# Optimization experiments

Hardware: AMD Instinct MI355X
Metric: run time of the kernel (lower is better)

Reference implementation:

```python
import jax, jax.numpy as jnp
import numpy as np

B, S, D, H, DH, TLEN, TD = 4, 1024, 1024, 16, 64, 256, 256
EPS = 1e-5


def layer_norm(x, g, b):
    m = jnp.mean(x, axis=-1, keepdims=True)
    v = jnp.mean((x - m) ** 2, axis=-1, keepdims=True)
    return (x - m) * jax.lax.rsqrt(v + EPS) * g + b


def rotate_half(x):
    x1, x2 = jnp.split(x, 2, axis=-1)
    return jnp.concatenate((-x2, x1), axis=-1)


def apply_rope(pos, t):
    # pos: [S, DH] -> [1, S, 1, DH]; t: [B, S, H, DH]
    p = pos[None, :, None, :]
    return t * jnp.cos(p) + rotate_half(t) * jnp.sin(p)


def mha(q_in, kv_in, in_w, in_b, out_w, out_b, n_heads):
    # standard nn.MultiheadAttention math (batch-first tensors here)
    d = q_in.shape[-1]
    dh = d // n_heads
    q = q_in @ in_w[:d].T + in_b[:d]
    k = kv_in @ in_w[d:2 * d].T + in_b[d:2 * d]
    v = kv_in @ in_w[2 * d:].T + in_b[2 * d:]
    q = q.reshape(q.shape[0], q.shape[1], n_heads, dh)
    k = k.reshape(k.shape[0], k.shape[1], n_heads, dh)
    v = v.reshape(v.shape[0], v.shape[1], n_heads, dh)
    scores = jnp.einsum('bihd,bjhd->bhij', q, k) / jnp.sqrt(jnp.asarray(dh, q.dtype))
    attn = jax.nn.softmax(scores, axis=-1)
    o = jnp.einsum('bhij,bjhd->bihd', attn, v)
    o = o.reshape(o.shape[0], o.shape[1], d)
    return o @ out_w.T + out_b


def setup_inputs():
    key = jax.random.key(0)
    ks = jax.random.split(key, 20)
    s = 0.02
    inp = {
        'x': jax.random.normal(ks[0], (B, S, D), jnp.float32),
        'text_emb': jax.random.normal(ks[1], (B, TLEN, D), jnp.float32),
        'time_emb': jax.random.normal(ks[2], (B, TD), jnp.float32),
    }
    # true RoPE position encoding, matching RotaryEmbedding.forward
    inv_freq = 1.0 / (10000 ** (jnp.arange(0, DH, 2, dtype=jnp.float32) / DH))
    freqs = jnp.arange(S, dtype=jnp.float32)[:, None] * inv_freq[None, :]
    inp['rotary_pos'] = jnp.concatenate((freqs, freqs), axis=-1)  # [S, DH]
    inp.update(
        ln1_g=jnp.ones((D,), jnp.float32), ln1_b=jnp.zeros((D,), jnp.float32),
        ln2_g=jnp.ones((D,), jnp.float32), ln2_b=jnp.zeros((D,), jnp.float32),
        ln3_g=jnp.ones((D,), jnp.float32), ln3_b=jnp.zeros((D,), jnp.float32),
        attn_in_w=jax.random.normal(ks[3], (3 * D, D), jnp.float32) * s,
        attn_in_b=jnp.zeros((3 * D,), jnp.float32),
        ca_in_w=jax.random.normal(ks[4], (3 * D, D), jnp.float32) * s,
        ca_in_b=jnp.zeros((3 * D,), jnp.float32),
        ca_out_w=jax.random.normal(ks[5], (D, D), jnp.float32) * s,
        ca_out_b=jnp.zeros((D,), jnp.float32),
        fc1_w=jax.random.normal(ks[6], (4 * D, D), jnp.float32) * s,
        fc1_b=jnp.zeros((4 * D,), jnp.float32),
        gate_w=jax.random.normal(ks[7], (4 * D, D), jnp.float32) * s,
        gate_b=jnp.zeros((4 * D,), jnp.float32),
        fc2_w=jax.random.normal(ks[8], (D, 4 * D), jnp.float32) * s,
        fc2_b=jnp.zeros((D,), jnp.float32),
    )
    return inp


def reference(x, text_emb, time_emb, rotary_pos,
              ln1_g, ln1_b, ln2_g, ln2_b, ln3_g, ln3_b,
              attn_in_w, attn_in_b,
              ca_in_w, ca_in_b, ca_out_w, ca_out_b,
              fc1_w, fc1_b, gate_w, gate_b, fc2_w, fc2_b):
    b, n, d = x.shape
    # --- self-attention with manual RoPE (NOTE: original skips out_proj) ---
    residual = x
    xn = layer_norm(x, ln1_g, ln1_b)
    q = xn @ attn_in_w[:d].T + attn_in_b[:d]
    k = xn @ attn_in_w[d:2 * d].T + attn_in_b[d:2 * d]
    v = xn @ attn_in_w[2 * d:].T + attn_in_b[2 * d:]
    q = q.reshape(b, n, H, DH)
    k = k.reshape(b, n, H, DH)
    v = v.reshape(b, n, H, DH)
    q = apply_rope(rotary_pos, q)
    k = apply_rope(rotary_pos, k)
    scores = jnp.einsum('bihd,bjhd->bhij', q, k) / jnp.sqrt(jnp.asarray(DH, x.dtype))
    attn = jax.nn.softmax(scores, axis=-1)
    attn_out = jnp.einsum('bhij,bjhd->bihd', attn, v).reshape(b, n, d)
    x = attn_out + residual
    # --- cross-attention (full MHA, dropout inactive at eval) ---
    residual = x
    xn = layer_norm(x, ln2_g, ln2_b)
    x = mha(xn, text_emb, ca_in_w, ca_in_b, ca_out_w, ca_out_b, H) + residual
    # --- gated MLP ---
    residual = x
    xn = layer_norm(x, ln3_g, ln3_b)
    h = jax.nn.gelu(xn @ fc1_w.T + fc1_b, approximate=False)
    g = jax.nn.sigmoid(xn @ gate_w.T + gate_b)
    return (h * g) @ fc2_w.T + fc2_b + residual
```

## Files before the change

kernel.cpp:

```cpp
#include <hip/hip_runtime.h>
#include <hip/hip_bf16.h>

#define SEQ 1024
#define DIM 1024
#define NH 16

typedef __bf16 bf16_t;
typedef __bf16 bf16x8 __attribute__((ext_vector_type(8)));
typedef __bf16 bf16x4 __attribute__((ext_vector_type(4)));
typedef float f32x4 __attribute__((ext_vector_type(4)));

__device__ __forceinline__ f32x4 mfma16(bf16x8 a, bf16x8 b, f32x4 c) {
    return __builtin_amdgcn_mfma_f32_16x16x32_bf16(a, b, c, 0, 0, 0);
}

__device__ __forceinline__ void gload16(const bf16_t* g, bf16_t* l) {
    __builtin_amdgcn_global_load_lds(
        (const __attribute__((address_space(1))) void*)g,
        (__attribute__((address_space(3))) void*)l, 16, 0, 0);
}

enum { EPI_BF16 = 0, EPI_F32_RESID = 1 };

__global__ __launch_bounds__(256) void cvt_kernel(const float* __restrict__ in,
                                                  bf16_t* __restrict__ out) {
    const int i = blockIdx.x * 256 + threadIdx.x;
    const float4 v = ((const float4*)in)[i];
    bf16x4 o = {(bf16_t)v.x, (bf16_t)v.y, (bf16_t)v.z, (bf16_t)v.w};
    ((bf16x4*)out)[i] = o;
}

__global__ __launch_bounds__(256) void ln_kernel(const float* __restrict__ in,
                                                 const float* __restrict__ g,
                                                 const float* __restrict__ bsh,
                                                 bf16_t* __restrict__ out) {
    __shared__ float red[4], red2[4];
    const int row = blockIdx.x, tid = threadIdx.x;
    const float4 v = ((const float4*)(in + (size_t)row * DIM))[tid];
    float s = v.x + v.y + v.z + v.w;
#pragma unroll
    for (int o = 32; o; o >>= 1) s += __shfl_down(s, o, 64);
    if ((tid & 63) == 0) red[tid >> 6] = s;
    __syncthreads();
    const float mean = (red[0] + red[1] + red[2] + red[3]) * (1.0f / DIM);
    const float dx = v.x - mean, dy = v.y - mean, dz = v.z - mean, dw = v.w - mean;
    float s2 = dx * dx + dy * dy + dz * dz + dw * dw;
#pragma unroll
    for (int o = 32; o; o >>= 1) s2 += __shfl_xor(s2, o, 64);
    if ((tid & 63) == 0) red2[tid >> 6] = s2;
    __syncthreads();
    const float var = (red2[0] + red2[1] + red2[2] + red2[3]) * (1.0f / DIM);
    const float rs = rsqrtf(var + 1e-5f);
    const float4 gv = ((const float4*)g)[tid];
    const float4 bv = ((const float4*)bsh)[tid];
    bf16x4 o4 = {(bf16_t)(dx * rs * gv.x + bv.x), (bf16_t)(dy * rs * gv.y + bv.y),
                 (bf16_t)(dz * rs * gv.z + bv.z), (bf16_t)(dw * rs * gv.w + bv.w)};
    ((bf16x4*)(out + (size_t)row * DIM))[tid] = o4;
}

__global__ __launch_bounds__(256) void rope_kernel(bf16_t* __restrict__ qkv,
                                                   const float* __restrict__ rp) {
    const int t = blockIdx.x * 256 + threadIdx.x;
    const int row = t >> 9;
    const int rem = t & 511;
    const int h = rem >> 5, d = rem & 31;
    const int s = row & (SEQ - 1);
    const float p0 = rp[s * 64 + d];
    const float p1 = rp[s * 64 + d + 32];
    float s0, c0, s1, c1;
    sincosf(p0, &s0, &c0);
    sincosf(p1, &s1, &c1);
    const size_t base = (size_t)row * 3072 + h * 64 + d;
#pragma unroll
    for (int off = 0; off <= 1024; off += 1024) {
        const float a = (float)qkv[base + off];
        const float b = (float)qkv[base + off + 32];
        qkv[base + off] = (bf16_t)(a * c0 - b * s0);
        qkv[base + off + 32] = (bf16_t)(b * c1 + a * s1);
    }
}

__device__ __forceinline__ float epi_apply_gelu(float v) {
    return 0.5f * v * (1.0f + erff(v * 0.70710678118f));
}

__global__ __launch_bounds__(256) void vtrans_kernel(
    const bf16_t* __restrict__ src, int ld, int voff, int skv,
    bf16_t* __restrict__ vt) {
    __shared__ bf16_t T[64 * 72];
    const int qt = blockIdx.x, h = blockIdx.y, b = blockIdx.z;
    const int tid = threadIdx.x;
    const int s0 = qt * 64;
#pragma unroll
    for (int t = 0; t < 2; ++t) {
        const int idx = t * 256 + tid;
        const int r = idx >> 3, c8 = (idx & 7) * 8;
        bf16x8 v = *(const bf16x8*)(src + (size_t)(b * skv + s0 + r) * ld +
                                    voff + h * 64 + c8);
        *(bf16x8*)&T[r * 72 + c8] = v;
    }
    __syncthreads();
    const size_t base = ((size_t)(b * NH + h) * 64) * skv;
#pragma unroll
    for (int t = 0; t < 2; ++t) {
        const int idx = t * 256 + tid;
        const int d = idx >> 3, s8 = (idx & 7) * 8;
        bf16x8 w;
#pragma unroll
        for (int i = 0; i < 8; ++i) w[i] = T[(s8 + i) * 72 + d];
        *(bf16x8*)(vt + base + (size_t)d * skv + s0 + s8) = w;
    }
}

#define ALD 72
template <bool OUTBF>
__global__ __launch_bounds__(256) void attn2_kernel(
    const bf16_t* __restrict__ qp, int ldq, int qoff,
    const bf16_t* __restrict__ kp, int ldk, int koff,
    const bf16_t* __restrict__ vtp, int skv,
    const float* __restrict__ resid, void* __restrict__ outp, float scale) {
    __shared__ bf16_t Ks[4096];
    __shared__ bf16_t Vs[4096];
    __shared__ bf16_t Ps[4 * 16 * ALD];
    const int nwg = gridDim.x;
    const int t = (blockIdx.x & 7) * (nwg >> 3) + (blockIdx.x >> 3);
    const int qt = t & 15;
    const int bh = t >> 4;
    const int b = bh >> 4, h = bh & 15;
    const int tid = threadIdx.x;
    const int wave = tid >> 6, lane = tid & 63;
    const int lr = lane & 15, hi = lane >> 4;

    const size_t qrow = (size_t)(b * SEQ + qt * 64 + wave * 16 + lr);
    const bf16_t* qb = qp + qrow * ldq + qoff + h * 64;
    const bf16x8 qf0 = *(const bf16x8*)(qb + hi * 8);
    const bf16x8 qf1 = *(const bf16x8*)(qb + 32 + hi * 8);

    const bf16_t* vbase = vtp + ((size_t)bh * 64) * skv;

    f32x4 oacc[4];
#pragma unroll
    for (int n = 0; n < 4; ++n) oacc[n] = (f32x4){0.f, 0.f, 0.f, 0.f};
    float mrun[4] = {-1e30f, -1e30f, -1e30f, -1e30f};
    float lrun[4] = {0.f, 0.f, 0.f, 0.f};

    bf16_t* pw = &Ps[wave * 16 * ALD];
    const int nkt = skv >> 6;
    for (int kt = 0; kt < nkt; ++kt) {
#pragma unroll
        for (int u = 0; u < 2; ++u) {
            const int c = wave * 2 + u;
            const int grow = wave * 16 + lr, gcol = u * 32 + hi * 8;
            gload16(kp + (size_t)(b * skv + kt * 64 + grow) * ldk + koff +
                        h * 64 + gcol,
                    &Ks[c * 512]);
            gload16(vbase + (size_t)grow * skv + kt * 64 + gcol, &Vs[c * 512]);
        }
        __syncthreads();

        f32x4 s[4];
#pragma unroll
        for (int n = 0; n < 4; ++n) {
            f32x4 z = (f32x4){0.f, 0.f, 0.f, 0.f};
            z = mfma16(qf0, *(const bf16x8*)&Ks[(n * 2 + 0) * 512 + hi * 128 + lr * 8], z);
            z = mfma16(qf1, *(const bf16x8*)&Ks[(n * 2 + 1) * 512 + hi * 128 + lr * 8], z);
            s[n] = z * scale;
        }
        float alpha[4];
#pragma unroll
        for (int j = 0; j < 4; ++j) {
            float mt = fmaxf(fmaxf(s[0][j], s[1][j]), fmaxf(s[2][j], s[3][j]));
#pragma unroll
            for (int o = 8; o >= 1; o >>= 1) mt = fmaxf(mt, __shfl_xor(mt, o, 64));
            const float mnew = fmaxf(mrun[j], mt);
            alpha[j] = __expf(mrun[j] - mnew);
            float rsum = 0.f;
#pragma unroll
            for (int n = 0; n < 4; ++n) {
                const float p = __expf(s[n][j] - mnew);
                s[n][j] = p;
                rsum += p;
            }
#pragma unroll
            for (int o = 8; o >= 1; o >>= 1) rsum += __shfl_xor(rsum, o, 64);
            lrun[j] = lrun[j] * alpha[j] + rsum;
            mrun[j] = mnew;
        }
#pragma unroll
        for (int j = 0; j < 4; ++j) {
            const int pr = hi * 4 + j;
#pragma unroll
            for (int n = 0; n < 4; ++n) pw[pr * ALD + n * 16 + lr] = (bf16_t)s[n][j];
        }
#pragma unroll
        for (int n = 0; n < 4; ++n)
#pragma unroll
            for (int j = 0; j < 4; ++j) oacc[n][j] *= alpha[j];
#pragma unroll
        for (int ks = 0; ks < 2; ++ks) {
            const bf16x8 pa = *(const bf16x8*)&pw[lr * ALD + ks * 32 + hi * 8];
#pragma unroll
            for (int n = 0; n < 4; ++n) {
                const bf16x8 vf =
                    *(const bf16x8*)&Vs[(n * 2 + ks) * 512 + hi * 128 + lr * 8];
                oacc[n] = mfma16(pa, vf, oacc[n]);
            }
        }
        __syncthreads();
    }

    const size_t orow0 = (size_t)(b * SEQ + qt * 64 + wave * 16);
#pragma unroll
    for (int n = 0; n < 4; ++n) {
#pragma unroll
        for (int j = 0; j < 4; ++j) {
            const int r = hi * 4 + j;
            const size_t idx = (orow0 + r) * DIM + h * 64 + n * 16 + lr;
            float val = oacc[n][j] / lrun[j];
            if constexpr (OUTBF) {
                ((bf16_t*)outp)[idx] = (bf16_t)val;
            } else {
                ((float*)outp)[idx] = val + resid[idx];
            }
        }
    }
}

template <int EPI, int MODE>
__global__ __launch_bounds__(512, 4) void gemm8w(
    const bf16_t* __restrict__ A, int lda, const bf16_t* __restrict__ W, int ldw,
    const float* __restrict__ bias, const void* __restrict__ aux,
    void* __restrict__ outv, int ldo, int K, int nM) {
    __shared__ bf16_t As[2][8192];
    __shared__ bf16_t Bs[2][8192];
    const int tid = threadIdx.x;
    const int wave = tid >> 6, lane = tid & 63;
    const int wm = wave >> 2, wn = wave & 3;
    const int lr = lane & 15, hi = lane >> 4;

    const int x = blockIdx.x & 7, i = blockIdx.x >> 3;
    int mt, nt;
    if constexpr (MODE == 0) {
        const int mc = nM >> 3;
        mt = x * mc + (i % mc);
        nt = i / mc;
    } else {
        const int nc = (gridDim.x / nM) >> 3;
        nt = x * nc + (i % nc);
        mt = i / nc;
    }
    const int rowA0 = mt * 128, rowB0 = nt * 128;

    f32x4 acc[4][2];
#pragma unroll
    for (int m = 0; m < 4; ++m)
#pragma unroll
        for (int n = 0; n < 2; ++n) acc[m][n] = (f32x4){0.f, 0.f, 0.f, 0.f};

    auto stage = [&](int kt, int b) {
        const int k0 = kt * 64;
#pragma unroll
        for (int u = 0; u < 2; ++u) {
            const int c = wave * 2 + u;
            const int grow = wave * 16 + lr, gcol = k0 + u * 32 + hi * 8;
            gload16(A + (size_t)(rowA0 + grow) * lda + gcol, &As[b][c * 512]);
            gload16(W + (size_t)(rowB0 + grow) * ldw + gcol, &Bs[b][c * 512]);
        }
    };

    const int NT = K >> 6;
    stage(0, 0);
    stage(1, 1);
    asm volatile("s_waitcnt vmcnt(4)" ::: "memory");
    __builtin_amdgcn_s_barrier();

    for (int kt = 0; kt < NT; ++kt) {
        const int cur = kt & 1;
#pragma unroll
        for (int ks = 0; ks < 2; ++ks) {
            bf16x8 af[4], bfr[2];
#pragma unroll
            for (int mf = 0; mf < 4; ++mf)
                af[mf] = *(const bf16x8*)&As[cur][((wm * 4 + mf) * 2 + ks) * 512 +
                                                 hi * 128 + lr * 8];
#pragma unroll
            for (int nf = 0; nf < 2; ++nf)
                bfr[nf] = *(const bf16x8*)&Bs[cur][((wn * 2 + nf) * 2 + ks) * 512 +
                                                  hi * 128 + lr * 8];
#pragma unroll
            for (int mf = 0; mf < 4; ++mf)
#pragma unroll
                for (int nf = 0; nf < 2; ++nf)
                    acc[mf][nf] = mfma16(af[mf], bfr[nf], acc[mf][nf]);
        }
        if (kt + 1 < NT) {
            __builtin_amdgcn_sched_barrier(0);
            __builtin_amdgcn_s_barrier();
            if (kt + 2 < NT) {
                stage(kt + 2, cur);
                asm volatile("s_waitcnt vmcnt(4)" ::: "memory");
            } else {
                asm volatile("s_waitcnt vmcnt(0)" ::: "memory");
            }
            __builtin_amdgcn_s_barrier();
        }
    }

    float bn[2];
#pragma unroll
    for (int n = 0; n < 2; ++n) bn[n] = bias[rowB0 + wn * 32 + n * 16 + lr];
#pragma unroll
    for (int m = 0; m < 4; ++m) {
#pragma unroll
        for (int j = 0; j < 4; ++j) {
            const int row = rowA0 + wm * 64 + m * 16 + hi * 4 + j;
#pragma unroll
            for (int n = 0; n < 2; ++n) {
                const int col = rowB0 + wn * 32 + n * 16 + lr;
                float val = acc[m][n][j] + bn[n];
                const size_t oidx = (size_t)row * ldo + col;
                if constexpr (EPI == EPI_BF16) {
                    ((bf16_t*)outv)[oidx] = (bf16_t)val;
                } else {
                    ((float*)outv)[oidx] = val + ((const float*)aux)[oidx];
                }
            }
        }
    }
}

__global__ __launch_bounds__(512, 4) void gemm_mlp(
    const bf16_t* __restrict__ A, int lda, const bf16_t* __restrict__ W1,
    const bf16_t* __restrict__ Wg, int ldw, const float* __restrict__ b1,
    const float* __restrict__ bg, bf16_t* __restrict__ outv, int ldo, int K,
    int nM) {
    __shared__ bf16_t As[2][8192];
    __shared__ bf16_t Bs[2][8192];
    const int tid = threadIdx.x;
    const int wave = tid >> 6, lane = tid & 63;
    const int wm = wave >> 2, wn = wave & 3;
    const int lr = lane & 15, hi = lane >> 4;

    const int x = blockIdx.x & 7, i = blockIdx.x >> 3;
    const int nc = (gridDim.x / nM) >> 3;
    const int nt = x * nc + (i % nc), mt = i / nc;
    const int rowA0 = mt * 128, colB0 = nt * 64;

    f32x4 acc[4][2];
#pragma unroll
    for (int m = 0; m < 4; ++m)
#pragma unroll
        for (int n = 0; n < 2; ++n) acc[m][n] = (f32x4){0.f, 0.f, 0.f, 0.f};

    const bf16_t* Wsrc = (wave & 1) ? Wg : W1;
    const int wrow = colB0 + (wave >> 1) * 16 + lr;
    auto stage = [&](int kt, int b) {
        const int k0 = kt * 64;
#pragma unroll
        for (int u = 0; u < 2; ++u) {
            const int c = wave * 2 + u;
            const int gcol = k0 + u * 32 + hi * 8;
            gload16(A + (size_t)(rowA0 + wave * 16 + lr) * lda + gcol,
                    &As[b][c * 512]);
            gload16(Wsrc + (size_t)wrow * ldw + gcol, &Bs[b][c * 512]);
        }
    };

    const int NT = K >> 6;
    stage(0, 0);
    stage(1, 1);
    asm volatile("s_waitcnt vmcnt(4)" ::: "memory");
    __builtin_amdgcn_s_barrier();

    for (int kt = 0; kt < NT; ++kt) {
        const int cur = kt & 1;
#pragma unroll
        for (int ks = 0; ks < 2; ++ks) {
            bf16x8 af[4], bh, bg_;
#pragma unroll
            for (int mf = 0; mf < 4; ++mf)
                af[mf] = *(const bf16x8*)&As[cur][((wm * 4 + mf) * 2 + ks) * 512 +
                                                 hi * 128 + lr * 8];
            bh = *(const bf16x8*)&Bs[cur][((2 * wn) * 2 + ks) * 512 + hi * 128 + lr * 8];
            bg_ = *(const bf16x8*)&Bs[cur][((2 * wn + 1) * 2 + ks) * 512 + hi * 128 + lr * 8];
#pragma unroll
            for (int mf = 0; mf < 4; ++mf) {
                acc[mf][0] = mfma16(af[mf], bh, acc[mf][0]);
                acc[mf][1] = mfma16(af[mf], bg_, acc[mf][1]);
            }
        }
        if (kt + 1 < NT) {
            __builtin_amdgcn_sched_barrier(0);
            __builtin_amdgcn_s_barrier();
            if (kt + 2 < NT) {
                stage(kt + 2, cur);
                asm volatile("s_waitcnt vmcnt(4)" ::: "memory");
            } else {
                asm volatile("s_waitcnt vmcnt(0)" ::: "memory");
            }
            __builtin_amdgcn_s_barrier();
        }
    }

    const int col = colB0 + wn * 16 + lr;
    const float bb1 = b1[col], bbg = bg[col];
#pragma unroll
    for (int m = 0; m < 4; ++m) {
#pragma unroll
        for (int j = 0; j < 4; ++j) {
            const int row = rowA0 + wm * 64 + m * 16 + hi * 4 + j;
            const float h = acc[m][0][j] + bb1;
            const float g = acc[m][1][j] + bbg;
            const float sg = 1.0f / (1.0f + __expf(-g));
            outv[(size_t)row * ldo + col] = (bf16_t)(epi_apply_gelu(h) * sg);
        }
    }
}

extern "C" void kernel_launch(void* const* d_in, const int* in_sizes, int n_in,
                              void* d_out, int out_size, void* d_ws, size_t ws_size,
                              hipStream_t stream) {
    const float* x = (const float*)d_in[0];
    const float* text_emb = (const float*)d_in[1];
    const float* rotary = (const float*)d_in[3];
    const float* ln1_g = (const float*)d_in[4];
    const float* ln1_b = (const float*)d_in[5];
    const float* ln2_g = (const float*)d_in[6];
    const float* ln2_b = (const float*)d_in[7];
    const float* ln3_g = (const float*)d_in[8];
    const float* ln3_b = (const float*)d_in[9];
    const float* attn_in_w = (const float*)d_in[10];
    const float* attn_in_b = (const float*)d_in[11];
    const float* ca_in_w = (const float*)d_in[12];
    const float* ca_in_b = (const float*)d_in[13];
    const float* ca_out_w = (const float*)d_in[14];
    const float* ca_out_b = (const float*)d_in[15];
    const float* fc1_w = (const float*)d_in[16];
    const float* fc1_b = (const float*)d_in[17];
    const float* gate_w = (const float*)d_in[18];
    const float* gate_b = (const float*)d_in[19];
    const float* fc2_w = (const float*)d_in[20];
    const float* fc2_b = (const float*)d_in[21];

    char* ws = (char*)d_ws;
    bf16_t* attn_w_bf = (bf16_t*)(ws);
    bf16_t* ca_in_bf = (bf16_t*)(ws + 6291456);
    bf16_t* ca_out_bf = (bf16_t*)(ws + 12582912);
    bf16_t* fc1_bf = (bf16_t*)(ws + 14680064);
    bf16_t* gate_bf = (bf16_t*)(ws + 23068672);
    bf16_t* fc2_bf = (bf16_t*)(ws + 31457280);
    bf16_t* text_bf = (bf16_t*)(ws + 39845888);
    bf16_t* xn = (bf16_t*)(ws + 41943040);
    float* xA = (float*)(ws + 50331648);
    char* S = ws + 67108864;
    bf16_t* qkv = (bf16_t*)S;
    bf16_t* vtSelf = (bf16_t*)(S + 25165824);
    bf16_t* cq = (bf16_t*)S;
    bf16_t* ckv = (bf16_t*)(S + 8388608);
    bf16_t* ca_attn = (bf16_t*)(S + 12582912);
    bf16_t* vtCross = (bf16_t*)(S + 20971520);
    bf16_t* hbuf = (bf16_t*)S;
    float* out = (float*)d_out;

    cvt_kernel<<<3072, 256, 0, stream>>>(attn_in_w, attn_w_bf);
    cvt_kernel<<<3072, 256, 0, stream>>>(ca_in_w, ca_in_bf);
    cvt_kernel<<<1024, 256, 0, stream>>>(ca_out_w, ca_out_bf);
    cvt_kernel<<<4096, 256, 0, stream>>>(fc1_w, fc1_bf);
    cvt_kernel<<<4096, 256, 0, stream>>>(gate_w, gate_bf);
    cvt_kernel<<<4096, 256, 0, stream>>>(fc2_w, fc2_bf);
    cvt_kernel<<<1024, 256, 0, stream>>>(text_emb, text_bf);

    ln_kernel<<<4096, 256, 0, stream>>>(x, ln1_g, ln1_b, xn);
    gemm8w<EPI_BF16, 0><<<768, 512, 0, stream>>>(
        xn, 1024, attn_w_bf, 1024, attn_in_b, nullptr, qkv, 3072, 1024, 32);
    rope_kernel<<<8192, 256, 0, stream>>>(qkv, rotary);
    vtrans_kernel<<<dim3(16, 16, 4), 256, 0, stream>>>(qkv, 3072, 2048, 1024, vtSelf);
    attn2_kernel<false><<<1024, 256, 0, stream>>>(
        qkv, 3072, 0, qkv, 3072, 1024, vtSelf, 1024, x, xA, 0.125f);

    ln_kernel<<<4096, 256, 0, stream>>>(xA, ln2_g, ln2_b, xn);
    gemm8w<EPI_BF16, 0><<<256, 512, 0, stream>>>(
        xn, 1024, ca_in_bf, 1024, ca_in_b, nullptr, cq, 1024, 1024, 32);
    gemm8w<EPI_BF16, 1><<<128, 512, 0, stream>>>(
        text_bf, 1024, ca_in_bf + (size_t)1024 * 1024, 1024, ca_in_b + 1024, nullptr,
        ckv, 2048, 1024, 8);
    vtrans_kernel<<<dim3(4, 16, 4), 256, 0, stream>>>(ckv, 2048, 1024, 256, vtCross);
    attn2_kernel<true><<<1024, 256, 0, stream>>>(
        cq, 1024, 0, ckv, 2048, 0, vtCross, 256, nullptr, ca_attn, 0.125f);
    gemm8w<EPI_F32_RESID, 0><<<256, 512, 0, stream>>>(
        ca_attn, 1024, ca_out_bf, 1024, ca_out_b, xA, xA, 1024, 1024, 32);

    ln_kernel<<<4096, 256, 0, stream>>>(xA, ln3_g, ln3_b, xn);
    gemm_mlp<<<2048, 512, 0, stream>>>(
        xn, 1024, fc1_bf, gate_bf, 1024, fc1_b, gate_b, hbuf, 4096, 1024, 32);
    gemm8w<EPI_F32_RESID, 0><<<256, 512, 0, stream>>>(
        hbuf, 4096, fc2_bf, 4096, fc2_b, xA, out, 1024, 4096, 32);
}
```

Baseline: 512.5 us.

## Switch GEMMs to 4-wave blocks with 64x64 warp tiles and K-step 32

Rewrites the 8-wave GEMM kernels as 4-wave (256-thread) blocks. Each wave now computes a 64x64 sub-tile (4x4 MFMA fragments) instead of 64x32, and the K step per stage drops from 64 to 32, which halves the LDS footprint. The MLP GEMM assigns the fc1 and gate halves to different wave pairs and exchanges the gate results through shared memory before the GELU*sigmoid epilogue. This raises register reuse per LDS read and lowers LDS use, at the cost of more register pressure, fewer waves per block to hide latency, and twice as many barrier iterations.

```diff
diff --git a/kernel.cpp b/kernel.cpp
--- a/kernel.cpp
+++ b/kernel.cpp
@@ -227,15 +227,15 @@
 }
 
 template <int EPI, int MODE>
-__global__ __launch_bounds__(512, 4) void gemm8w(
+__global__ __launch_bounds__(256, 3) void gemm4w(
     const bf16_t* __restrict__ A, int lda, const bf16_t* __restrict__ W, int ldw,
     const float* __restrict__ bias, const void* __restrict__ aux,
     void* __restrict__ outv, int ldo, int K, int nM) {
-    __shared__ bf16_t As[2][8192];
-    __shared__ bf16_t Bs[2][8192];
+    __shared__ bf16_t As[2][4096];
+    __shared__ bf16_t Bs[2][4096];
     const int tid = threadIdx.x;
     const int wave = tid >> 6, lane = tid & 63;
-    const int wm = wave >> 2, wn = wave & 3;
+    const int wm = wave >> 1, wn = wave & 1;
     const int lr = lane & 15, hi = lane >> 4;
 
     const int x = blockIdx.x & 7, i = blockIdx.x >> 3;
@@ -251,24 +251,25 @@
     }
     const int rowA0 = mt * 128, rowB0 = nt * 128;
 
-    f32x4 acc[4][2];
+    f32x4 acc[4][4];
 #pragma unroll
     for (int m = 0; m < 4; ++m)
 #pragma unroll
-        for (int n = 0; n < 2; ++n) acc[m][n] = (f32x4){0.f, 0.f, 0.f, 0.f};
+        for (int n = 0; n < 4; ++n) acc[m][n] = (f32x4){0.f, 0.f, 0.f, 0.f};
 
     auto stage = [&](int kt, int b) {
-        const int k0 = kt * 64;
+        const int k0 = kt * 32;
+        const int gcol = k0 + hi * 8;
 #pragma unroll
         for (int u = 0; u < 2; ++u) {
             const int c = wave * 2 + u;
-            const int grow = wave * 16 + lr, gcol = k0 + u * 32 + hi * 8;
+            const int grow = c * 16 + lr;
             gload16(A + (size_t)(rowA0 + grow) * lda + gcol, &As[b][c * 512]);
             gload16(W + (size_t)(rowB0 + grow) * ldw + gcol, &Bs[b][c * 512]);
         }
     };
 
-    const int NT = K >> 6;
+    const int NT = K >> 5;
     stage(0, 0);
     stage(1, 1);
     asm volatile("s_waitcnt vmcnt(4)" ::: "memory");
@@ -276,23 +277,18 @@
 
     for (int kt = 0; kt < NT; ++kt) {
         const int cur = kt & 1;
-#pragma unroll
-        for (int ks = 0; ks < 2; ++ks) {
-            bf16x8 af[4], bfr[2];
-#pragma unroll
-            for (int mf = 0; mf < 4; ++mf)
-                af[mf] = *(const bf16x8*)&As[cur][((wm * 4 + mf) * 2 + ks) * 512 +
-                                                 hi * 128 + lr * 8];
-#pragma unroll
-            for (int nf = 0; nf < 2; ++nf)
-                bfr[nf] = *(const bf16x8*)&Bs[cur][((wn * 2 + nf) * 2 + ks) * 512 +
-                                                  hi * 128 + lr * 8];
-#pragma unroll
-            for (int mf = 0; mf < 4; ++mf)
-#pragma unroll
-                for (int nf = 0; nf < 2; ++nf)
-                    acc[mf][nf] = mfma16(af[mf], bfr[nf], acc[mf][nf]);
-        }
+        bf16x8 af[4], bfr[4];
+#pragma unroll
+        for (int mf = 0; mf < 4; ++mf)
+            af[mf] = *(const bf16x8*)&As[cur][(wm * 4 + mf) * 512 + hi * 128 + lr * 8];
+#pragma unroll
+        for (int nf = 0; nf < 4; ++nf)
+            bfr[nf] = *(const bf16x8*)&Bs[cur][(wn * 4 + nf) * 512 + hi * 128 + lr * 8];
+#pragma unroll
+        for (int mf = 0; mf < 4; ++mf)
+#pragma unroll
+            for (int nf = 0; nf < 4; ++nf)
+                acc[mf][nf] = mfma16(af[mf], bfr[nf], acc[mf][nf]);
         if (kt + 1 < NT) {
             __builtin_amdgcn_sched_barrier(0);
             __builtin_amdgcn_s_barrier();
@@ -306,17 +302,17 @@
         }
     }
 
-    float bn[2];
-#pragma unroll
-    for (int n = 0; n < 2; ++n) bn[n] = bias[rowB0 + wn * 32 + n * 16 + lr];
+    float bn[4];
+#pragma unroll
+    for (int n = 0; n < 4; ++n) bn[n] = bias[rowB0 + wn * 64 + n * 16 + lr];
 #pragma unroll
     for (int m = 0; m < 4; ++m) {
 #pragma unroll
         for (int j = 0; j < 4; ++j) {
             const int row = rowA0 + wm * 64 + m * 16 + hi * 4 + j;
 #pragma unroll
-            for (int n = 0; n < 2; ++n) {
-                const int col = rowB0 + wn * 32 + n * 16 + lr;
+            for (int n = 0; n < 4; ++n) {
+                const int col = rowB0 + wn * 64 + n * 16 + lr;
                 float val = acc[m][n][j] + bn[n];
                 const size_t oidx = (size_t)row * ldo + col;
                 if constexpr (EPI == EPI_BF16) {
@@ -329,16 +325,18 @@
     }
 }
 
-__global__ __launch_bounds__(512, 4) void gemm_mlp(
+__global__ __launch_bounds__(256, 3) void gemm_mlp(
     const bf16_t* __restrict__ A, int lda, const bf16_t* __restrict__ W1,
     const bf16_t* __restrict__ Wg, int ldw, const float* __restrict__ b1,
     const float* __restrict__ bg, bf16_t* __restrict__ outv, int ldo, int K,
     int nM) {
-    __shared__ bf16_t As[2][8192];
-    __shared__ bf16_t Bs[2][8192];
+    __shared__ __align__(16) char smem[32768];
+    auto As = (bf16_t(*)[4096])smem;
+    auto Bs = (bf16_t(*)[4096])(smem + 16384);
+    float* gx = (float*)smem;
     const int tid = threadIdx.x;
     const int wave = tid >> 6, lane = tid & 63;
-    const int wm = wave >> 2, wn = wave & 3;
+    const int role = wave >> 1, wm = wave & 1;
     const int lr = lane & 15, hi = lane >> 4;
 
     const int x = blockIdx.x & 7, i = blockIdx.x >> 3;
@@ -346,27 +344,26 @@
     const int nt = x * nc + (i % nc), mt = i / nc;
     const int rowA0 = mt * 128, colB0 = nt * 64;
 
-    f32x4 acc[4][2];
+    f32x4 acc[4][4];
 #pragma unroll
     for (int m = 0; m < 4; ++m)
 #pragma unroll
-        for (int n = 0; n < 2; ++n) acc[m][n] = (f32x4){0.f, 0.f, 0.f, 0.f};
-
-    const bf16_t* Wsrc = (wave & 1) ? Wg : W1;
-    const int wrow = colB0 + (wave >> 1) * 16 + lr;
+        for (int n = 0; n < 4; ++n) acc[m][n] = (f32x4){0.f, 0.f, 0.f, 0.f};
+
     auto stage = [&](int kt, int b) {
-        const int k0 = kt * 64;
+        const int k0 = kt * 32;
+        const int gcol = k0 + hi * 8;
 #pragma unroll
         for (int u = 0; u < 2; ++u) {
             const int c = wave * 2 + u;
-            const int gcol = k0 + u * 32 + hi * 8;
-            gload16(A + (size_t)(rowA0 + wave * 16 + lr) * lda + gcol,
-                    &As[b][c * 512]);
+            gload16(A + (size_t)(rowA0 + c * 16 + lr) * lda + gcol, &As[b][c * 512]);
+            const bf16_t* Wsrc = (c < 4) ? W1 : Wg;
+            const int wrow = colB0 + (c & 3) * 16 + lr;
             gload16(Wsrc + (size_t)wrow * ldw + gcol, &Bs[b][c * 512]);
         }
     };
 
-    const int NT = K >> 6;
+    const int NT = K >> 5;
     stage(0, 0);
     stage(1, 1);
     asm volatile("s_waitcnt vmcnt(4)" ::: "memory");
@@ -374,21 +371,18 @@
 
     for (int kt = 0; kt < NT; ++kt) {
         const int cur = kt & 1;
-#pragma unroll
-        for (int ks = 0; ks < 2; ++ks) {
-            bf16x8 af[4], bh, bg_;
-#pragma unroll
-            for (int mf = 0; mf < 4; ++mf)
-                af[mf] = *(const bf16x8*)&As[cur][((wm * 4 + mf) * 2 + ks) * 512 +
-                                                 hi * 128 + lr * 8];
-            bh = *(const bf16x8*)&Bs[cur][((2 * wn) * 2 + ks) * 512 + hi * 128 + lr * 8];
-            bg_ = *(const bf16x8*)&Bs[cur][((2 * wn + 1) * 2 + ks) * 512 + hi * 128 + lr * 8];
-#pragma unroll
-            for (int mf = 0; mf < 4; ++mf) {
-                acc[mf][0] = mfma16(af[mf], bh, acc[mf][0]);
-                acc[mf][1] = mfma16(af[mf], bg_, acc[mf][1]);
-            }
-        }
+        bf16x8 af[4], bfr[4];
+#pragma unroll
+        for (int mf = 0; mf < 4; ++mf)
+            af[mf] = *(const bf16x8*)&As[cur][(wm * 4 + mf) * 512 + hi * 128 + lr * 8];
+#pragma unroll
+        for (int nf = 0; nf < 4; ++nf)
+            bfr[nf] = *(const bf16x8*)&Bs[cur][(role * 4 + nf) * 512 + hi * 128 + lr * 8];
+#pragma unroll
+        for (int mf = 0; mf < 4; ++mf)
+#pragma unroll
+            for (int nf = 0; nf < 4; ++nf)
+                acc[mf][nf] = mfma16(af[mf], bfr[nf], acc[mf][nf]);
         if (kt + 1 < NT) {
             __builtin_amdgcn_sched_barrier(0);
             __builtin_amdgcn_s_barrier();
@@ -402,17 +396,36 @@
         }
     }
 
-    const int col = colB0 + wn * 16 + lr;
-    const float bb1 = b1[col], bbg = bg[col];
-#pragma unroll
-    for (int m = 0; m < 4; ++m) {
-#pragma unroll
-        for (int j = 0; j < 4; ++j) {
-            const int row = rowA0 + wm * 64 + m * 16 + hi * 4 + j;
-            const float h = acc[m][0][j] + bb1;
-            const float g = acc[m][1][j] + bbg;
-            const float sg = 1.0f / (1.0f + __expf(-g));
-            outv[(size_t)row * ldo + col] = (bf16_t)(epi_apply_gelu(h) * sg);
+    __syncthreads();
+    if (role == 1) {
+#pragma unroll
+        for (int m = 0; m < 4; ++m)
+#pragma unroll
+            for (int j = 0; j < 4; ++j) {
+                const int r = wm * 64 + m * 16 + hi * 4 + j;
+#pragma unroll
+                for (int n = 0; n < 4; ++n)
+                    gx[r * 64 + n * 16 + lr] =
+                        acc[m][n][j] + bg[colB0 + n * 16 + lr];
+            }
+    }
+    __syncthreads();
+    if (role == 0) {
+#pragma unroll
+        for (int m = 0; m < 4; ++m) {
+#pragma unroll
+            for (int j = 0; j < 4; ++j) {
+                const int r = wm * 64 + m * 16 + hi * 4 + j;
+                const int row = rowA0 + r;
+#pragma unroll
+                for (int n = 0; n < 4; ++n) {
+                    const int col = colB0 + n * 16 + lr;
+                    const float h = acc[m][n][j] + b1[col];
+                    const float g = gx[r * 64 + n * 16 + lr];
+                    const float sg = 1.0f / (1.0f + __expf(-g));
+                    outv[(size_t)row * ldo + col] = (bf16_t)(epi_apply_gelu(h) * sg);
+                }
+            }
         }
     }
 }
@@ -471,7 +484,7 @@
     cvt_kernel<<<1024, 256, 0, stream>>>(text_emb, text_bf);
 
     ln_kernel<<<4096, 256, 0, stream>>>(x, ln1_g, ln1_b, xn);
-    gemm8w<EPI_BF16, 0><<<768, 512, 0, stream>>>(
+    gemm4w<EPI_BF16, 0><<<768, 256, 0, stream>>>(
         xn, 1024, attn_w_bf, 1024, attn_in_b, nullptr, qkv, 3072, 1024, 32);
     rope_kernel<<<8192, 256, 0, stream>>>(qkv, rotary);
     vtrans_kernel<<<dim3(16, 16, 4), 256, 0, stream>>>(qkv, 3072, 2048, 1024, vtSelf);
@@ -479,20 +492,20 @@
         qkv, 3072, 0, qkv, 3072, 1024, vtSelf, 1024, x, xA, 0.125f);
 
     ln_kernel<<<4096, 256, 0, stream>>>(xA, ln2_g, ln2_b, xn);
-    gemm8w<EPI_BF16, 0><<<256, 512, 0, stream>>>(
+    gemm4w<EPI_BF16, 0><<<256, 256, 0, stream>>>(
         xn, 1024, ca_in_bf, 1024, ca_in_b, nullptr, cq, 1024, 1024, 32);
-    gemm8w<EPI_BF16, 1><<<128, 512, 0, stream>>>(
+    gemm4w<EPI_BF16, 1><<<128, 256, 0, stream>>>(
         text_bf, 1024, ca_in_bf + (size_t)1024 * 1024, 1024, ca_in_b + 1024, nullptr,
         ckv, 2048, 1024, 8);
     vtrans_kernel<<<dim3(4, 16, 4), 256, 0, stream>>>(ckv, 2048, 1024, 256, vtCross);
     attn2_kernel<true><<<1024, 256, 0, stream>>>(
         cq, 1024, 0, ckv, 2048, 0, vtCross, 256, nullptr, ca_attn, 0.125f);
-    gemm8w<EPI_F32_RESID, 0><<<256, 512, 0, stream>>>(
+    gemm4w<EPI_F32_RESID, 0><<<256, 256, 0, stream>>>(
         ca_attn, 1024, ca_out_bf, 1024, ca_out_b, xA, xA, 1024, 1024, 32);
 
     ln_kernel<<<4096, 256, 0, stream>>>(xA, ln3_g, ln3_b, xn);
-    gemm_mlp<<<2048, 512, 0, stream>>>(
+    gemm_mlp<<<2048, 256, 0, stream>>>(
         xn, 1024, fc1_bf, gate_bf, 1024, fc1_b, gate_b, hbuf, 4096, 1024, 32);
-    gemm8w<EPI_F32_RESID, 0><<<256, 512, 0, stream>>>(
+    gemm4w<EPI_F32_RESID, 0><<<256, 256, 0, stream>>>(
         hbuf, 4096, fc2_bf, 4096, fc2_b, xA, out, 1024, 4096, 32);
 }
```

Result: slower. 527.6 us (+2.9%).

## Switch GEMMs to 4-stage K=32 LDS pipeline with single barrier per step

Applied to the files above, without the earlier changes.

Both GEMM kernels move from a double-buffered K=64 tile to a four-buffer ring of K=32 tiles, prefetching three steps ahead. The loads for step kt+3 are issued before the MFMAs of step kt, and the loop now uses one barrier per iteration instead of two. The aim is to hide global-to-LDS latency better and cut synchronization stalls. In exchange there are twice as many iterations, each with half the MFMA work per barrier. Reusing a ring slot right after the barrier needs the wait counts to stay correct.

```diff
diff --git a/kernel.cpp b/kernel.cpp
--- a/kernel.cpp
+++ b/kernel.cpp
@@ -227,12 +227,12 @@
 }
 
 template <int EPI, int MODE>
-__global__ __launch_bounds__(512, 4) void gemm8w(
+__global__ __launch_bounds__(512, 4) void gemm8d(
     const bf16_t* __restrict__ A, int lda, const bf16_t* __restrict__ W, int ldw,
     const float* __restrict__ bias, const void* __restrict__ aux,
     void* __restrict__ outv, int ldo, int K, int nM) {
-    __shared__ bf16_t As[2][8192];
-    __shared__ bf16_t Bs[2][8192];
+    __shared__ bf16_t As[4][4096];
+    __shared__ bf16_t Bs[4][4096];
     const int tid = threadIdx.x;
     const int wave = tid >> 6, lane = tid & 63;
     const int wm = wave >> 2, wn = wave & 3;
@@ -258,50 +258,44 @@
         for (int n = 0; n < 2; ++n) acc[m][n] = (f32x4){0.f, 0.f, 0.f, 0.f};
 
     auto stage = [&](int kt, int b) {
-        const int k0 = kt * 64;
-#pragma unroll
-        for (int u = 0; u < 2; ++u) {
-            const int c = wave * 2 + u;
-            const int grow = wave * 16 + lr, gcol = k0 + u * 32 + hi * 8;
-            gload16(A + (size_t)(rowA0 + grow) * lda + gcol, &As[b][c * 512]);
-            gload16(W + (size_t)(rowB0 + grow) * ldw + gcol, &Bs[b][c * 512]);
-        }
+        const int k0 = kt * 32;
+        const int gcol = k0 + hi * 8;
+        const int grow = wave * 16 + lr;
+        gload16(A + (size_t)(rowA0 + grow) * lda + gcol, &As[b][wave * 512]);
+        gload16(W + (size_t)(rowB0 + grow) * ldw + gcol, &Bs[b][wave * 512]);
     };
 
-    const int NT = K >> 6;
+    const int NT = K >> 5;
     stage(0, 0);
     stage(1, 1);
+    stage(2, 2);
     asm volatile("s_waitcnt vmcnt(4)" ::: "memory");
     __builtin_amdgcn_s_barrier();
 
     for (int kt = 0; kt < NT; ++kt) {
-        const int cur = kt & 1;
-#pragma unroll
-        for (int ks = 0; ks < 2; ++ks) {
-            bf16x8 af[4], bfr[2];
-#pragma unroll
-            for (int mf = 0; mf < 4; ++mf)
-                af[mf] = *(const bf16x8*)&As[cur][((wm * 4 + mf) * 2 + ks) * 512 +
-                                                 hi * 128 + lr * 8];
+        const int cur = kt & 3;
+        if (kt + 3 < NT) stage(kt + 3, (kt + 3) & 3);
+        __builtin_amdgcn_sched_barrier(0);
+        bf16x8 af[4], bfr[2];
+#pragma unroll
+        for (int mf = 0; mf < 4; ++mf)
+            af[mf] = *(const bf16x8*)&As[cur][(wm * 4 + mf) * 512 + lane * 8];
+#pragma unroll
+        for (int nf = 0; nf < 2; ++nf)
+            bfr[nf] = *(const bf16x8*)&Bs[cur][(wn * 2 + nf) * 512 + lane * 8];
+#pragma unroll
+        for (int mf = 0; mf < 4; ++mf)
 #pragma unroll
             for (int nf = 0; nf < 2; ++nf)
-                bfr[nf] = *(const bf16x8*)&Bs[cur][((wn * 2 + nf) * 2 + ks) * 512 +
-                                                  hi * 128 + lr * 8];
-#pragma unroll
-            for (int mf = 0; mf < 4; ++mf)
-#pragma unroll
-                for (int nf = 0; nf < 2; ++nf)
-                    acc[mf][nf] = mfma16(af[mf], bfr[nf], acc[mf][nf]);
-        }
+                acc[mf][nf] = mfma16(af[mf], bfr[nf], acc[mf][nf]);
+        __builtin_amdgcn_sched_barrier(0);
         if (kt + 1 < NT) {
-            __builtin_amdgcn_sched_barrier(0);
-            __builtin_amdgcn_s_barrier();
-            if (kt + 2 < NT) {
-                stage(kt + 2, cur);
+            if (kt + 3 < NT)
                 asm volatile("s_waitcnt vmcnt(4)" ::: "memory");
-            } else {
+            else if (kt + 2 < NT)
+                asm volatile("s_waitcnt vmcnt(2)" ::: "memory");
+            else
                 asm volatile("s_waitcnt vmcnt(0)" ::: "memory");
-            }
             __builtin_amdgcn_s_barrier();
         }
     }
@@ -329,13 +323,13 @@
     }
 }
 
-__global__ __launch_bounds__(512, 4) void gemm_mlp(
+__global__ __launch_bounds__(512, 4) void gemm_mlp_d(
     const bf16_t* __restrict__ A, int lda, const bf16_t* __restrict__ W1,
     const bf16_t* __restrict__ Wg, int ldw, const float* __restrict__ b1,
     const float* __restrict__ bg, bf16_t* __restrict__ outv, int ldo, int K,
     int nM) {
-    __shared__ bf16_t As[2][8192];
-    __shared__ bf16_t Bs[2][8192];
+    __shared__ bf16_t As[4][4096];
+    __shared__ bf16_t Bs[4][4096];
     const int tid = threadIdx.x;
     const int wave = tid >> 6, lane = tid & 63;
     const int wm = wave >> 2, wn = wave & 3;
@@ -352,52 +346,46 @@
 #pragma unroll
         for (int n = 0; n < 2; ++n) acc[m][n] = (f32x4){0.f, 0.f, 0.f, 0.f};
 
-    const bf16_t* Wsrc = (wave & 1) ? Wg : W1;
-    const int wrow = colB0 + (wave >> 1) * 16 + lr;
+    const bf16_t* Wsrc = (wave < 4) ? W1 : Wg;
+    const int wrow = colB0 + (wave & 3) * 16 + lr;
     auto stage = [&](int kt, int b) {
-        const int k0 = kt * 64;
-#pragma unroll
-        for (int u = 0; u < 2; ++u) {
-            const int c = wave * 2 + u;
-            const int gcol = k0 + u * 32 + hi * 8;
-            gload16(A + (size_t)(rowA0 + wave * 16 + lr) * lda + gcol,
-                    &As[b][c * 512]);
-            gload16(Wsrc + (size_t)wrow * ldw + gcol, &Bs[b][c * 512]);
-        }
+        const int k0 = kt * 32;
+        const int gcol = k0 + hi * 8;
+        gload16(A + (size_t)(rowA0 + wave * 16 + lr) * lda + gcol,
+                &As[b][wave * 512]);
+        gload16(Wsrc + (size_t)wrow * ldw + gcol, &Bs[b][wave * 512]);
     };
 
-    const int NT = K >> 6;
+    const int NT = K >> 5;
     stage(0, 0);
     stage(1, 1);
+    stage(2, 2);
     asm volatile("s_waitcnt vmcnt(4)" ::: "memory");
     __builtin_amdgcn_s_barrier();
 
     for (int kt = 0; kt < NT; ++kt) {
-        const int cur = kt & 1;
-#pragma unroll
-        for (int ks = 0; ks < 2; ++ks) {
-            bf16x8 af[4], bh, bg_;
-#pragma unroll
-            for (int mf = 0; mf < 4; ++mf)
-                af[mf] = *(const bf16x8*)&As[cur][((wm * 4 + mf) * 2 + ks) * 512 +
-                                                 hi * 128 + lr * 8];
-            bh = *(const bf16x8*)&Bs[cur][((2 * wn) * 2 + ks) * 512 + hi * 128 + lr * 8];
-            bg_ = *(const bf16x8*)&Bs[cur][((2 * wn + 1) * 2 + ks) * 512 + hi * 128 + lr * 8];
-#pragma unroll
-            for (int mf = 0; mf < 4; ++mf) {
-                acc[mf][0] = mfma16(af[mf], bh, acc[mf][0]);
-                acc[mf][1] = mfma16(af[mf], bg_, acc[mf][1]);
-            }
-        }
+        const int cur = kt & 3;
+        if (kt + 3 < NT) stage(kt + 3, (kt + 3) & 3);
+        __builtin_amdgcn_sched_barrier(0);
+        bf16x8 af[4], bh, bg_;
+#pragma unroll
+        for (int mf = 0; mf < 4; ++mf)
+            af[mf] = *(const bf16x8*)&As[cur][(wm * 4 + mf) * 512 + lane * 8];
+        bh = *(const bf16x8*)&Bs[cur][wn * 512 + lane * 8];
+        bg_ = *(const bf16x8*)&Bs[cur][(4 + wn) * 512 + lane * 8];
+#pragma unroll
+        for (int mf = 0; mf < 4; ++mf) {
+            acc[mf][0] = mfma16(af[mf], bh, acc[mf][0]);
+            acc[mf][1] = mfma16(af[mf], bg_, acc[mf][1]);
+        }
+        __builtin_amdgcn_sched_barrier(0);
         if (kt + 1 < NT) {
-            __builtin_amdgcn_sched_barrier(0);
-            __builtin_amdgcn_s_barrier();
-            if (kt + 2 < NT) {
-                stage(kt + 2, cur);
+            if (kt + 3 < NT)
                 asm volatile("s_waitcnt vmcnt(4)" ::: "memory");
-            } else {
+            else if (kt + 2 < NT)
+                asm volatile("s_waitcnt vmcnt(2)" ::: "memory");
+            else
                 asm volatile("s_waitcnt vmcnt(0)" ::: "memory");
-            }
             __builtin_amdgcn_s_barrier();
         }
     }
@@ -471,7 +459,7 @@
     cvt_kernel<<<1024, 256, 0, stream>>>(text_emb, text_bf);
 
     ln_kernel<<<4096, 256, 0, stream>>>(x, ln1_g, ln1_b, xn);
-    gemm8w<EPI_BF16, 0><<<768, 512, 0, stream>>>(
+    gemm8d<EPI_BF16, 0><<<768, 512, 0, stream>>>(
         xn, 1024, attn_w_bf, 1024, attn_in_b, nullptr, qkv, 3072, 1024, 32);
     rope_kernel<<<8192, 256, 0, stream>>>(qkv, rotary);
     vtrans_kernel<<<dim3(16, 16, 4), 256, 0, stream>>>(qkv, 3072, 2048, 1024, vtSelf);
@@ -479,20 +467,20 @@
         qkv, 3072, 0, qkv, 3072, 1024, vtSelf, 1024, x, xA, 0.125f);
 
     ln_kernel<<<4096, 256, 0, stream>>>(xA, ln2_g, ln2_b, xn);
-    gemm8w<EPI_BF16, 0><<<256, 512, 0, stream>>>(
+    gemm8d<EPI_BF16, 0><<<256, 512, 0, stream>>>(
         xn, 1024, ca_in_bf, 1024, ca_in_b, nullptr, cq, 1024, 1024, 32);
-    gemm8w<EPI_BF16, 1><<<128, 512, 0, stream>>>(
+    gemm8d<EPI_BF16, 1><<<128, 512, 0, stream>>>(
         text_bf, 1024, ca_in_bf + (size_t)1024 * 1024, 1024, ca_in_b + 1024, nullptr,
         ckv, 2048, 1024, 8);
     vtrans_kernel<<<dim3(4, 16, 4), 256, 0, stream>>>(ckv, 2048, 1024, 256, vtCross);
     attn2_kernel<true><<<1024, 256, 0, stream>>>(
         cq, 1024, 0, ckv, 2048, 0, vtCross, 256, nullptr, ca_attn, 0.125f);
-    gemm8w<EPI_F32_RESID, 0><<<256, 512, 0, stream>>>(
+    gemm8d<EPI_F32_RESID, 0><<<256, 512, 0, stream>>>(
         ca_attn, 1024, ca_out_bf, 1024, ca_out_b, xA, xA, 1024, 1024, 32);
 
     ln_kernel<<<4096, 256, 0, stream>>>(xA, ln3_g, ln3_b, xn);
-    gemm_mlp<<<2048, 512, 0, stream>>>(
+    gemm_mlp_d<<<2048, 512, 0, stream>>>(
         xn, 1024, fc1_bf, gate_bf, 1024, fc1_b, gate_b, hbuf, 4096, 1024, 32);
-    gemm8w<EPI_F32_RESID, 0><<<256, 512, 0, stream>>>(
+    gemm8d<EPI_F32_RESID, 0><<<256, 512, 0, stream>>>(
         hbuf, 4096, fc2_bf, 4096, fc2_b, xA, out, 1024, 4096, 32);
 }
```

After: 540.8 us. 5.5% more time.
